# Performance work log

Measured on AMD Instinct MI355X. Metric: run time of the kernel, lower is better.

## Reference

```python
import jax, jax.numpy as jnp
import numpy as np

EPS = 1e-6
NEG = -1e9
RES_RATIO = 1.0  # res_ratio init arg
MAKE_SYM = True


def _ln(x, g, b):
    m = jnp.mean(x, axis=-1, keepdims=True)
    v = jnp.mean((x - m) ** 2, axis=-1, keepdims=True)
    return (x - m) * jax.lax.rsqrt(v + EPS) * g + b


def _sim(q, k, W1q, W1k, b1, W2, b2):
    # NN(concat([q,k])) with first dense split into query/key halves:
    # relu(q@W1q + k@W1k + b1) @ W2 + b2  -> avoids materializing the 2d concat.
    qa = q @ W1q  # [b,n,sq,h]
    kb = k @ W1k  # [b,n,sk,h]
    h1 = jax.nn.relu(qa[:, :, :, None, :] + kb[:, :, None, :, :] + b1)  # [b,n,sq,sk,h]
    s = jnp.einsum('bnqkh,h->bnqk', h1, W2[:, 0]) + b2[0]
    if MAKE_SYM:
        qb = q @ W1k
        ka = k @ W1q
        h2 = jax.nn.relu(ka[:, :, None, :, :] + qb[:, :, :, None, :] + b1)
        s = s + jnp.einsum('bnqkh,h->bnqk', h2, W2[:, 0]) + b2[0]
    return s


def _attention(v, k, q, mask, Ww, bw, Wd, bd, W1q, W1k, b1, W2, b2):
    q = q @ Ww + bw
    k = k @ Ww + bw
    v = v @ Ww + bw
    logits = _sim(q, k, W1q, W1k, b1, W2, b2)
    if mask is not None:
        logits = logits + mask * NEG
    attn = jax.nn.softmax(logits, axis=-1)
    out = jnp.einsum('bnqk,bnkd->bnqd', attn, v)
    return out @ Wd + bd, attn


def setup_inputs() -> dict:
    key = jax.random.key(0)
    B, N, S, D, DFF, H = 4, 1, 256, 128, 512, 128
    ks = jax.random.split(key, 16)
    s = 0.02
    inp = {
        'x': jax.random.normal(ks[0], (B, N, S, D), jnp.float32),
        'enc_output': jax.random.normal(ks[1], (B, N, S, D), jnp.float32),
        'com_mask': jnp.zeros((B, N, S, S), jnp.float32),
        'dec_mask': jnp.zeros((B, N, S, S), jnp.float32),
        # shared pairwise-score MLP NN: Dense(H, relu) -> Dense(1)
        'W1q': jax.random.normal(ks[2], (D, H), jnp.float32) * s,
        'W1k': jax.random.normal(ks[3], (D, H), jnp.float32) * s,
        'b1': jnp.zeros((H,), jnp.float32),
        'W2': jax.random.normal(ks[4], (H, 1), jnp.float32) * s,
        'b2': jnp.zeros((1,), jnp.float32),
        # mha1 projections
        'Ww1': jax.random.normal(ks[5], (D, D), jnp.float32) * s,
        'bw1': jnp.zeros((D,), jnp.float32),
        'Wd1': jax.random.normal(ks[6], (D, D), jnp.float32) * s,
        'bd1': jnp.zeros((D,), jnp.float32),
        # mha2 projections
        'Ww2': jax.random.normal(ks[7], (D, D), jnp.float32) * s,
        'bw2': jnp.zeros((D,), jnp.float32),
        'Wd2': jax.random.normal(ks[8], (D, D), jnp.float32) * s,
        'bd2': jnp.zeros((D,), jnp.float32),
        # ffn
        'Wf1': jax.random.normal(ks[9], (D, DFF), jnp.float32) * s,
        'bf1': jnp.zeros((DFF,), jnp.float32),
        'Wf2': jax.random.normal(ks[10], (DFF, D), jnp.float32) * s,
        'bf2': jnp.zeros((D,), jnp.float32),
        # layernorms
        'ln1_g': jnp.ones((D,), jnp.float32), 'ln1_b': jnp.zeros((D,), jnp.float32),
        'ln2_g': jnp.ones((D,), jnp.float32), 'ln2_b': jnp.zeros((D,), jnp.float32),
        'ln3_g': jnp.ones((D,), jnp.float32), 'ln3_b': jnp.zeros((D,), jnp.float32),
    }
    return inp


def reference(x, enc_output, com_mask, dec_mask,
              W1q, W1k, b1, W2, b2,
              Ww1, bw1, Wd1, bd1,
              Ww2, bw2, Wd2, bd2,
              Wf1, bf1, Wf2, bf2,
              ln1_g, ln1_b, ln2_g, ln2_b, ln3_g, ln3_b):
    r = RES_RATIO
    # self-attention block (dropout inactive, eval mode)
    attn1, aw1 = _attention(x, x, x, com_mask, Ww1, bw1, Wd1, bd1, W1q, W1k, b1, W2, b2)
    out1 = _ln((2 - r) * attn1 + r * x, ln1_g, ln1_b)
    # cross-attention block
    attn2, aw2 = _attention(enc_output, enc_output, out1, dec_mask, Ww2, bw2, Wd2, bd2, W1q, W1k, b1, W2, b2)
    out2 = _ln((2 - r) * attn2 + r * out1, ln2_g, ln2_b)
    # ffn
    ffn = jax.nn.relu(out2 @ Wf1 + bf1) @ Wf2 + bf2
    out3 = _ln((2 - r) * ffn + r * out2, ln3_g, ln3_b)
    return out3
```

## Files before the change

kernel.cpp:

```cpp
#include <hip/hip_runtime.h>
#include <math.h>


#define LN_EPS 1e-6f
#define NEGV  (-1e9f)

constexpr int B = 4, S = 256, D = 128, H = 128, DFF = 512;
constexpr int R = B * S;
constexpr int LDW = H + 4;

struct P {
    const float *x, *enc, *com_mask, *dec_mask;
    const float *W1q, *W1k, *b1, *W2;
    const float *Ww1, *bw1, *Wd1, *bd1;
    const float *Ww2, *bw2, *Wd2, *bd2;
    const float *Wf1, *bf1, *Wf2, *bf2;
    const float *ln1g, *ln1b, *ln2g, *ln2b, *ln3g, *ln3b;
    float *out;
    float *xw, *qa, *kb, *kv2w, *kb2, *ka2, *qa2, *qb2;
    float *sbuf, *sbuf2, *out1, *out2;
};

__device__ __forceinline__ float4 mm8(const float* AshS, const float* W,
                                      const float* bias, int lr, int c4)
{
    const float4* W4 = (const float4*)W;
    float4 acc = bias ? ((const float4*)bias)[c4] : make_float4(0.f, 0.f, 0.f, 0.f);
    #pragma unroll 8
    for (int k = 0; k < 128; ++k) {
        const float a = AshS[lr * 128 + k];
        const float4 w = W4[k * 32 + c4];
        acc.x = fmaf(a, w.x, acc.x); acc.y = fmaf(a, w.y, acc.y);
        acc.z = fmaf(a, w.z, acc.z); acc.w = fmaf(a, w.w, acc.w);
    }
    return acc;
}

__global__ __launch_bounds__(256) void proj3_kernel(P p)
{
    const int g = blockIdx.y, tid = threadIdx.x;
    const int r0 = blockIdx.x * 8;
    const int lr = tid >> 5, c4 = tid & 31;
    __shared__ float Ash[8 * 128];
    __shared__ float Pw[8 * 128];

    const float* A    = g ? p.enc  : p.x;
    const float* Wp   = g ? p.Ww2  : p.Ww1;
    const float* bp   = g ? p.bw2  : p.bw1;
    float*       o_w  = g ? p.kv2w : p.xw;
    const float* Wsec = g ? p.W1k  : p.W1q;
    const float* bsec = g ? nullptr: p.b1;
    float*       o_s  = g ? p.kb2  : p.qa;
    const float* Wthr = g ? p.W1q  : p.W1k;
    float*       o_t  = g ? p.ka2  : p.kb;

    ((float4*)Ash)[tid] = ((const float4*)(A + (size_t)r0 * 128))[tid];
    __syncthreads();
    {
        const float4 w = mm8(Ash, Wp, bp, lr, c4);
        ((float4*)(Pw + lr * 128))[c4] = w;
        ((float4*)o_w)[(size_t)(r0 + lr) * 32 + c4] = w;
    }
    __syncthreads();
    {
        const float4 q = mm8(Pw, Wsec, bsec, lr, c4);
        ((float4*)o_s)[(size_t)(r0 + lr) * 32 + c4] = q;
        const float4 k = mm8(Pw, Wthr, nullptr, lr, c4);
        ((float4*)o_t)[(size_t)(r0 + lr) * 32 + c4] = k;
    }
}

#define PW_STEP(AP0, AP1, BP0, BP1)                                            \
    {                                                                          \
        const float4 w  = *(const float4*)(W2s + h);                           \
        const float4 a0 = *(const float4*)((AP0) + h);                         \
        const float4 a1 = *(const float4*)((AP1) + h);                         \
        const float4 b0 = *(const float4*)((BP0) + h);                         \
        const float4 b1 = *(const float4*)((BP1) + h);                         \
        acc00 = fmaf(fmaxf(a0.x+b0.x,0.f),w.x,acc00); acc00 = fmaf(fmaxf(a0.y+b0.y,0.f),w.y,acc00); \
        acc00 = fmaf(fmaxf(a0.z+b0.z,0.f),w.z,acc00); acc00 = fmaf(fmaxf(a0.w+b0.w,0.f),w.w,acc00); \
        acc01 = fmaf(fmaxf(a0.x+b1.x,0.f),w.x,acc01); acc01 = fmaf(fmaxf(a0.y+b1.y,0.f),w.y,acc01); \
        acc01 = fmaf(fmaxf(a0.z+b1.z,0.f),w.z,acc01); acc01 = fmaf(fmaxf(a0.w+b1.w,0.f),w.w,acc01); \
        acc10 = fmaf(fmaxf(a1.x+b0.x,0.f),w.x,acc10); acc10 = fmaf(fmaxf(a1.y+b0.y,0.f),w.y,acc10); \
        acc10 = fmaf(fmaxf(a1.z+b0.z,0.f),w.z,acc10); acc10 = fmaf(fmaxf(a1.w+b0.w,0.f),w.w,acc10); \
        acc11 = fmaf(fmaxf(a1.x+b1.x,0.f),w.x,acc11); acc11 = fmaf(fmaxf(a1.y+b1.y,0.f),w.y,acc11); \
        acc11 = fmaf(fmaxf(a1.z+b1.z,0.f),w.z,acc11); acc11 = fmaf(fmaxf(a1.w+b1.w,0.f),w.w,acc11); \
    }

__global__ __launch_bounds__(256) void pairwise_self_kernel(P p)
{
    __shared__ __align__(16) float As[32 * LDW];
    __shared__ __align__(16) float Bs[32 * LDW];
    __shared__ __align__(16) float W2s[H];
    const int b = blockIdx.z, q0 = blockIdx.y * 32, k0 = blockIdx.x * 32;
    const int tid = threadIdx.x, bS = b * S;
    for (int i = tid; i < 32 * (H / 4); i += 256) {
        const int r = i >> 5, c4 = i & 31;
        ((float4*)(As + r * LDW))[c4] = ((const float4*)(p.qa + (size_t)(bS + q0 + r) * H))[c4];
        ((float4*)(Bs + r * LDW))[c4] = ((const float4*)(p.kb + (size_t)(bS + k0 + r) * H))[c4];
    }
    if (tid < H / 4) ((float4*)W2s)[tid] = ((const float4*)p.W2)[tid];
    __syncthreads();
    const int tx = tid & 15, ty = tid >> 4;
    const float* A0 = As + (2 * ty) * LDW; const float* A1 = A0 + LDW;
    const float* B0 = Bs + (2 * tx) * LDW; const float* B1 = B0 + LDW;
    float acc00 = 0.f, acc01 = 0.f, acc10 = 0.f, acc11 = 0.f;
    #pragma unroll 4
    for (int h = 0; h < H; h += 4) PW_STEP(A0, A1, B0, B1);
    const size_t base = (size_t)(bS + q0 + 2 * ty) * S + (k0 + 2 * tx);
    *(float2*)(p.sbuf + base)     = make_float2(acc00, acc01);
    *(float2*)(p.sbuf + base + S) = make_float2(acc10, acc11);
}

__global__ __launch_bounds__(256) void pairwise_cross2_kernel(P p)
{
    __shared__ __align__(16) float As[32 * LDW];
    __shared__ __align__(16) float Bs[32 * LDW];
    __shared__ __align__(16) float W2s[H];
    const int b = blockIdx.z, q0 = blockIdx.y * 32, k0 = blockIdx.x * 32;
    const int tid = threadIdx.x, bS = b * S;
    const int tx = tid & 15, ty = tid >> 4;
    const float* A0 = As + (2 * ty) * LDW; const float* A1 = A0 + LDW;
    const float* B0 = Bs + (2 * tx) * LDW; const float* B1 = B0 + LDW;
    float acc00 = 0.f, acc01 = 0.f, acc10 = 0.f, acc11 = 0.f;

    for (int i = tid; i < 32 * (H / 4); i += 256) {
        const int r = i >> 5, c4 = i & 31;
        ((float4*)(As + r * LDW))[c4] = ((const float4*)(p.qa2 + (size_t)(bS + q0 + r) * H))[c4];
        ((float4*)(Bs + r * LDW))[c4] = ((const float4*)(p.kb2 + (size_t)(bS + k0 + r) * H))[c4];
    }
    if (tid < H / 4) ((float4*)W2s)[tid] = ((const float4*)p.W2)[tid];
    __syncthreads();
    #pragma unroll 4
    for (int h = 0; h < H; h += 4) PW_STEP(A0, A1, B0, B1);
    __syncthreads();
    for (int i = tid; i < 32 * (H / 4); i += 256) {
        const int r = i >> 5, c4 = i & 31;
        ((float4*)(As + r * LDW))[c4] = ((const float4*)(p.qb2 + (size_t)(bS + q0 + r) * H))[c4];
        ((float4*)(Bs + r * LDW))[c4] = ((const float4*)(p.ka2 + (size_t)(bS + k0 + r) * H))[c4];
    }
    __syncthreads();
    #pragma unroll 4
    for (int h = 0; h < H; h += 4) PW_STEP(A0, A1, B0, B1);
    const size_t base = (size_t)(bS + q0 + 2 * ty) * S + (k0 + 2 * tx);
    *(float2*)(p.sbuf2 + base)     = make_float2(acc00, acc01);
    *(float2*)(p.sbuf2 + base + S) = make_float2(acc10, acc11);
}

template<bool SYM, bool QPROJ>
__global__ __launch_bounds__(256) void attn_tail_kernel(P p)
{
    __shared__ float s8[8 * 256];
    __shared__ float aoS[8 * 128];
    __shared__ float o1S[8 * 128];
    const float* Sin  = SYM ? p.sbuf : p.sbuf2;
    const float* mask = SYM ? p.com_mask : p.dec_mask;
    const float* V    = SYM ? p.xw : p.kv2w;
    const float* Wd   = SYM ? p.Wd1 : p.Wd2;
    const float* bd   = SYM ? p.bd1 : p.bd2;
    const float* res  = SYM ? p.x : p.out1;
    const float* lg   = SYM ? p.ln1g : p.ln2g;
    const float* lb   = SYM ? p.ln1b : p.ln2b;
    float* outp       = SYM ? p.out1 : p.out2;

    const int tid = threadIdx.x;
    const int r0 = blockIdx.x * 8, b = r0 >> 8, bS = b * S;

    for (int i = tid; i < 8 * 256; i += 256) {
        const int r = i >> 8, k = i & 255;
        const int row = r0 + r, q = row & 255;
        float l = Sin[(size_t)row * S + k];
        if (SYM) l += Sin[(size_t)(bS + k) * S + q];
        l += mask[(size_t)row * S + k] * NEGV;
        s8[i] = l;
    }
    __syncthreads();
    {
        const int g = tid >> 5, c = tid & 31;
        float* rowp = s8 + g * 256;
        float m = -INFINITY;
        for (int k = c; k < 256; k += 32) m = fmaxf(m, rowp[k]);
        for (int o = 16; o; o >>= 1) m = fmaxf(m, __shfl_xor(m, o, 32));
        float s = 0.f;
        for (int k = c; k < 256; k += 32) { const float e = __expf(rowp[k] - m); rowp[k] = e; s += e; }
        for (int o = 16; o; o >>= 1) s += __shfl_xor(s, o, 32);
        const float rinv = 1.f / s;
        for (int k = c; k < 256; k += 32) rowp[k] *= rinv;
    }
    __syncthreads();
    const int lr = tid >> 5, c4 = tid & 31;
    {
        const float4* V4 = (const float4*)(V + (size_t)bS * D);
        float4 acc = make_float4(0.f, 0.f, 0.f, 0.f);
        #pragma unroll 8
        for (int k = 0; k < 256; ++k) {
            const float a = s8[lr * 256 + k];
            const float4 v = V4[k * 32 + c4];
            acc.x = fmaf(a, v.x, acc.x); acc.y = fmaf(a, v.y, acc.y);
            acc.z = fmaf(a, v.z, acc.z); acc.w = fmaf(a, v.w, acc.w);
        }
        ((float4*)(aoS + lr * 128))[c4] = acc;
    }
    __syncthreads();
    {
        float4 o = mm8(aoS, Wd, bd, lr, c4);
        const float4 r4 = ((const float4*)(res + (size_t)(r0 + lr) * 128))[c4];
        const float x0 = o.x + r4.x, x1 = o.y + r4.y, x2 = o.z + r4.z, x3 = o.w + r4.w;
        float s  = x0 + x1 + x2 + x3;
        float s2 = x0 * x0 + x1 * x1 + x2 * x2 + x3 * x3;
        for (int of = 16; of; of >>= 1) { s += __shfl_xor(s, of, 32); s2 += __shfl_xor(s2, of, 32); }
        const float m = s * (1.f / 128), var = s2 * (1.f / 128) - m * m;
        const float rs = rsqrtf(var + LN_EPS);
        const float4 gv = ((const float4*)lg)[c4], bv = ((const float4*)lb)[c4];
        float4 o4;
        o4.x = (x0 - m) * rs * gv.x + bv.x; o4.y = (x1 - m) * rs * gv.y + bv.y;
        o4.z = (x2 - m) * rs * gv.z + bv.z; o4.w = (x3 - m) * rs * gv.w + bv.w;
        ((float4*)outp)[(size_t)(r0 + lr) * 32 + c4] = o4;
        if (QPROJ) { ((float4*)(o1S + lr * 128))[c4] = o4; }
    }
    if (QPROJ) {
        __syncthreads();
        const float4 w = mm8(o1S, p.Ww2, p.bw2, lr, c4);
        ((float4*)(aoS + lr * 128))[c4] = w;
        __syncthreads();
        const float4 q = mm8(aoS, p.W1q, p.b1, lr, c4);
        ((float4*)p.qa2)[(size_t)(r0 + lr) * 32 + c4] = q;
        const float4 k = mm8(aoS, p.W1k, p.b1, lr, c4);
        ((float4*)p.qb2)[(size_t)(r0 + lr) * 32 + c4] = k;
    }
}

__global__ __launch_bounds__(256) void ffn_kernel(P p)
{
    __shared__ float o2S[4 * 128];
    __shared__ float hidP[2 * 4 * 512];
    __shared__ float part[8 * 4 * 128];
    const int r0 = blockIdx.x * 4, tid = threadIdx.x;

    if (tid < 128) ((float4*)o2S)[tid] = ((const float4*)(p.out2 + (size_t)r0 * 128))[tid];
    __syncthreads();

    {
        const int c4 = tid & 127, kh = tid >> 7;
        const float4* Wf1_4 = (const float4*)p.Wf1;
        float4 a0 = make_float4(0.f,0.f,0.f,0.f), a1 = a0, a2 = a0, a3 = a0;
        const int kbase = kh * 64;
        #pragma unroll 8
        for (int k = 0; k < 64; ++k) {
            const int kk = kbase + k;
            const float4 w = Wf1_4[kk * 128 + c4];
            const float s0 = o2S[kk], s1 = o2S[128 + kk], s2 = o2S[256 + kk], s3 = o2S[384 + kk];
            a0.x = fmaf(s0, w.x, a0.x); a0.y = fmaf(s0, w.y, a0.y); a0.z = fmaf(s0, w.z, a0.z); a0.w = fmaf(s0, w.w, a0.w);
            a1.x = fmaf(s1, w.x, a1.x); a1.y = fmaf(s1, w.y, a1.y); a1.z = fmaf(s1, w.z, a1.z); a1.w = fmaf(s1, w.w, a1.w);
            a2.x = fmaf(s2, w.x, a2.x); a2.y = fmaf(s2, w.y, a2.y); a2.z = fmaf(s2, w.z, a2.z); a2.w = fmaf(s2, w.w, a2.w);
            a3.x = fmaf(s3, w.x, a3.x); a3.y = fmaf(s3, w.y, a3.y); a3.z = fmaf(s3, w.z, a3.z); a3.w = fmaf(s3, w.w, a3.w);
        }
        float4* h4 = (float4*)(hidP + kh * 2048);
        h4[0 * 128 + c4] = a0; h4[1 * 128 + c4] = a1;
        h4[2 * 128 + c4] = a2; h4[3 * 128 + c4] = a3;
    }
    __syncthreads();
    for (int i = tid; i < 2048; i += 256) {
        const int c = i & 511;
        hidP[i] = fmaxf(hidP[i] + hidP[2048 + i] + p.bf1[c], 0.f);
    }
    __syncthreads();

    {
        const int c4 = tid & 31, kg = tid >> 5;
        const float4* Wf2_4 = (const float4*)p.Wf2;
        float4 a0 = make_float4(0.f,0.f,0.f,0.f), a1 = a0, a2 = a0, a3 = a0;
        const int kbase = kg * 64;
        #pragma unroll 8
        for (int k = 0; k < 64; ++k) {
            const int kk = kbase + k;
            const float4 w = Wf2_4[kk * 32 + c4];
            const float s0 = hidP[kk], s1 = hidP[512 + kk], s2 = hidP[1024 + kk], s3 = hidP[1536 + kk];
            a0.x = fmaf(s0, w.x, a0.x); a0.y = fmaf(s0, w.y, a0.y); a0.z = fmaf(s0, w.z, a0.z); a0.w = fmaf(s0, w.w, a0.w);
            a1.x = fmaf(s1, w.x, a1.x); a1.y = fmaf(s1, w.y, a1.y); a1.z = fmaf(s1, w.z, a1.z); a1.w = fmaf(s1, w.w, a1.w);
            a2.x = fmaf(s2, w.x, a2.x); a2.y = fmaf(s2, w.y, a2.y); a2.z = fmaf(s2, w.z, a2.z); a2.w = fmaf(s2, w.w, a2.w);
            a3.x = fmaf(s3, w.x, a3.x); a3.y = fmaf(s3, w.y, a3.y); a3.z = fmaf(s3, w.z, a3.z); a3.w = fmaf(s3, w.w, a3.w);
        }
        float4* p4 = (float4*)part;
        p4[(kg * 4 + 0) * 32 + c4] = a0; p4[(kg * 4 + 1) * 32 + c4] = a1;
        p4[(kg * 4 + 2) * 32 + c4] = a2; p4[(kg * 4 + 3) * 32 + c4] = a3;
    }
    __syncthreads();

    if (tid < 128) {
        const int row = tid >> 5, c4 = tid & 31;
        const float4* p4 = (const float4*)part;
        float4 sum = ((const float4*)p.bf2)[c4];
        #pragma unroll
        for (int kg = 0; kg < 8; ++kg) {
            const float4 v = p4[(kg * 4 + row) * 32 + c4];
            sum.x += v.x; sum.y += v.y; sum.z += v.z; sum.w += v.w;
        }
        const float4 r4 = ((const float4*)o2S)[row * 32 + c4];
        const float x0 = sum.x + r4.x, x1 = sum.y + r4.y, x2 = sum.z + r4.z, x3 = sum.w + r4.w;
        float s  = x0 + x1 + x2 + x3;
        float s2 = x0 * x0 + x1 * x1 + x2 * x2 + x3 * x3;
        for (int of = 16; of; of >>= 1) { s += __shfl_xor(s, of, 32); s2 += __shfl_xor(s2, of, 32); }
        const float m = s * (1.f / 128), var = s2 * (1.f / 128) - m * m;
        const float rs = rsqrtf(var + LN_EPS);
        const float4 gv = ((const float4*)p.ln3g)[c4], bv = ((const float4*)p.ln3b)[c4];
        float4 o4;
        o4.x = (x0 - m) * rs * gv.x + bv.x; o4.y = (x1 - m) * rs * gv.y + bv.y;
        o4.z = (x2 - m) * rs * gv.z + bv.z; o4.w = (x3 - m) * rs * gv.w + bv.w;
        ((float4*)p.out)[(size_t)(r0 + row) * 32 + c4] = o4;
    }
}

extern "C" void kernel_launch(void* const* d_in, const int* in_sizes, int n_in,
                              void* d_out, int out_size, void* d_ws, size_t ws_size,
                              hipStream_t stream) {
    (void)in_sizes; (void)n_in; (void)out_size; (void)ws_size;
    P p;
    p.x        = (const float*)d_in[0];
    p.enc      = (const float*)d_in[1];
    p.com_mask = (const float*)d_in[2];
    p.dec_mask = (const float*)d_in[3];
    p.W1q = (const float*)d_in[4];
    p.W1k = (const float*)d_in[5];
    p.b1  = (const float*)d_in[6];
    p.W2  = (const float*)d_in[7];
    p.Ww1 = (const float*)d_in[9];
    p.bw1 = (const float*)d_in[10];
    p.Wd1 = (const float*)d_in[11];
    p.bd1 = (const float*)d_in[12];
    p.Ww2 = (const float*)d_in[13];
    p.bw2 = (const float*)d_in[14];
    p.Wd2 = (const float*)d_in[15];
    p.bd2 = (const float*)d_in[16];
    p.Wf1 = (const float*)d_in[17];
    p.bf1 = (const float*)d_in[18];
    p.Wf2 = (const float*)d_in[19];
    p.bf2 = (const float*)d_in[20];
    p.ln1g = (const float*)d_in[21];
    p.ln1b = (const float*)d_in[22];
    p.ln2g = (const float*)d_in[23];
    p.ln2b = (const float*)d_in[24];
    p.ln3g = (const float*)d_in[25];
    p.ln3b = (const float*)d_in[26];
    p.out  = (float*)d_out;

    float* ws = (float*)d_ws;
    const size_t RD  = (size_t)R * D;
    const size_t SSz = (size_t)B * S * S;
    p.xw    = ws;
    p.qa    = p.xw    + RD;
    p.kb    = p.qa    + RD;
    p.kv2w  = p.kb    + RD;
    p.kb2   = p.kv2w  + RD;
    p.ka2   = p.kb2   + RD;
    p.qa2   = p.ka2   + RD;
    p.qb2   = p.qa2   + RD;
    p.sbuf  = p.qb2   + RD;
    p.sbuf2 = p.sbuf  + SSz;
    p.out1  = p.sbuf2 + SSz;
    p.out2  = p.out1  + RD;

    proj3_kernel<<<dim3(R / 8, 2), 256, 0, stream>>>(p);
    pairwise_self_kernel<<<dim3(8, 8, 4), 256, 0, stream>>>(p);
    attn_tail_kernel<true, true><<<R / 8, 256, 0, stream>>>(p);
    pairwise_cross2_kernel<<<dim3(8, 8, 4), 256, 0, stream>>>(p);
    attn_tail_kernel<false, false><<<R / 8, 256, 0, stream>>>(p);
    ffn_kernel<<<R / 4, 256, 0, stream>>>(p);
}
```

Measured before the change: 199.0 us.

## Fuse pairwise scoring, softmax tail and FFN into per-row attention kernels

Merges the pairwise score kernels into the attention tail kernels, so each block of 8 query rows computes its logits against all 256 keys in shared memory. K tiles are register-prefetched one step ahead. The symmetric term is computed directly from the transposed projections rather than by reading the score transpose back from global memory, and the FFN plus its layernorm moves into the cross-attention kernel. This drops the score buffers and three launches. The catch is lower parallelism: 128 blocks, each recomputing against the full key set, with a small per-thread tile and no register blocking in the pairwise loop.

```diff
diff --git a/kernel.cpp b/kernel.cpp
--- a/kernel.cpp
+++ b/kernel.cpp
@@ -17,8 +17,7 @@
     const float *Wf1, *bf1, *Wf2, *bf2;
     const float *ln1g, *ln1b, *ln2g, *ln2b, *ln3g, *ln3b;
     float *out;
-    float *xw, *qa, *kb, *kv2w, *kb2, *ka2, *qa2, *qb2;
-    float *sbuf, *sbuf2, *out1, *out2;
+    float *xw, *qa, *kb, *kv2w, *kb2, *ka2, *qa2, *qb2, *out1;
 };
 
 __device__ __forceinline__ float4 mm8(const float* AshS, const float* W,
@@ -70,116 +69,106 @@
     }
 }
 
-#define PW_STEP(AP0, AP1, BP0, BP1)                                            \
-    {                                                                          \
-        const float4 w  = *(const float4*)(W2s + h);                           \
-        const float4 a0 = *(const float4*)((AP0) + h);                         \
-        const float4 a1 = *(const float4*)((AP1) + h);                         \
-        const float4 b0 = *(const float4*)((BP0) + h);                         \
-        const float4 b1 = *(const float4*)((BP1) + h);                         \
-        acc00 = fmaf(fmaxf(a0.x+b0.x,0.f),w.x,acc00); acc00 = fmaf(fmaxf(a0.y+b0.y,0.f),w.y,acc00); \
-        acc00 = fmaf(fmaxf(a0.z+b0.z,0.f),w.z,acc00); acc00 = fmaf(fmaxf(a0.w+b0.w,0.f),w.w,acc00); \
-        acc01 = fmaf(fmaxf(a0.x+b1.x,0.f),w.x,acc01); acc01 = fmaf(fmaxf(a0.y+b1.y,0.f),w.y,acc01); \
-        acc01 = fmaf(fmaxf(a0.z+b1.z,0.f),w.z,acc01); acc01 = fmaf(fmaxf(a0.w+b1.w,0.f),w.w,acc01); \
-        acc10 = fmaf(fmaxf(a1.x+b0.x,0.f),w.x,acc10); acc10 = fmaf(fmaxf(a1.y+b0.y,0.f),w.y,acc10); \
-        acc10 = fmaf(fmaxf(a1.z+b0.z,0.f),w.z,acc10); acc10 = fmaf(fmaxf(a1.w+b0.w,0.f),w.w,acc10); \
-        acc11 = fmaf(fmaxf(a1.x+b1.x,0.f),w.x,acc11); acc11 = fmaf(fmaxf(a1.y+b1.y,0.f),w.y,acc11); \
-        acc11 = fmaf(fmaxf(a1.z+b1.z,0.f),w.z,acc11); acc11 = fmaf(fmaxf(a1.w+b1.w,0.f),w.w,acc11); \
-    }
-
-__global__ __launch_bounds__(256) void pairwise_self_kernel(P p)
+template<bool CROSS>
+__global__ __launch_bounds__(256) void attn_fused(P p)
 {
-    __shared__ __align__(16) float As[32 * LDW];
-    __shared__ __align__(16) float Bs[32 * LDW];
-    __shared__ __align__(16) float W2s[H];
-    const int b = blockIdx.z, q0 = blockIdx.y * 32, k0 = blockIdx.x * 32;
-    const int tid = threadIdx.x, bS = b * S;
-    for (int i = tid; i < 32 * (H / 4); i += 256) {
-        const int r = i >> 5, c4 = i & 31;
-        ((float4*)(As + r * LDW))[c4] = ((const float4*)(p.qa + (size_t)(bS + q0 + r) * H))[c4];
-        ((float4*)(Bs + r * LDW))[c4] = ((const float4*)(p.kb + (size_t)(bS + k0 + r) * H))[c4];
-    }
-    if (tid < H / 4) ((float4*)W2s)[tid] = ((const float4*)p.W2)[tid];
-    __syncthreads();
-    const int tx = tid & 15, ty = tid >> 4;
-    const float* A0 = As + (2 * ty) * LDW; const float* A1 = A0 + LDW;
-    const float* B0 = Bs + (2 * tx) * LDW; const float* B1 = B0 + LDW;
-    float acc00 = 0.f, acc01 = 0.f, acc10 = 0.f, acc11 = 0.f;
-    #pragma unroll 4
-    for (int h = 0; h < H; h += 4) PW_STEP(A0, A1, B0, B1);
-    const size_t base = (size_t)(bS + q0 + 2 * ty) * S + (k0 + 2 * tx);
-    *(float2*)(p.sbuf + base)     = make_float2(acc00, acc01);
-    *(float2*)(p.sbuf + base + S) = make_float2(acc10, acc11);
-}
-
-__global__ __launch_bounds__(256) void pairwise_cross2_kernel(P p)
-{
-    __shared__ __align__(16) float As[32 * LDW];
-    __shared__ __align__(16) float Bs[32 * LDW];
-    __shared__ __align__(16) float W2s[H];
-    const int b = blockIdx.z, q0 = blockIdx.y * 32, k0 = blockIdx.x * 32;
-    const int tid = threadIdx.x, bS = b * S;
-    const int tx = tid & 15, ty = tid >> 4;
-    const float* A0 = As + (2 * ty) * LDW; const float* A1 = A0 + LDW;
-    const float* B0 = Bs + (2 * tx) * LDW; const float* B1 = B0 + LDW;
-    float acc00 = 0.f, acc01 = 0.f, acc10 = 0.f, acc11 = 0.f;
-
-    for (int i = tid; i < 32 * (H / 4); i += 256) {
-        const int r = i >> 5, c4 = i & 31;
-        ((float4*)(As + r * LDW))[c4] = ((const float4*)(p.qa2 + (size_t)(bS + q0 + r) * H))[c4];
-        ((float4*)(Bs + r * LDW))[c4] = ((const float4*)(p.kb2 + (size_t)(bS + k0 + r) * H))[c4];
-    }
-    if (tid < H / 4) ((float4*)W2s)[tid] = ((const float4*)p.W2)[tid];
-    __syncthreads();
-    #pragma unroll 4
-    for (int h = 0; h < H; h += 4) PW_STEP(A0, A1, B0, B1);
-    __syncthreads();
-    for (int i = tid; i < 32 * (H / 4); i += 256) {
-        const int r = i >> 5, c4 = i & 31;
-        ((float4*)(As + r * LDW))[c4] = ((const float4*)(p.qb2 + (size_t)(bS + q0 + r) * H))[c4];
-        ((float4*)(Bs + r * LDW))[c4] = ((const float4*)(p.ka2 + (size_t)(bS + k0 + r) * H))[c4];
-    }
-    __syncthreads();
-    #pragma unroll 4
-    for (int h = 0; h < H; h += 4) PW_STEP(A0, A1, B0, B1);
-    const size_t base = (size_t)(bS + q0 + 2 * ty) * S + (k0 + 2 * tx);
-    *(float2*)(p.sbuf2 + base)     = make_float2(acc00, acc01);
-    *(float2*)(p.sbuf2 + base + S) = make_float2(acc10, acc11);
-}
-
-template<bool SYM, bool QPROJ>
-__global__ __launch_bounds__(256) void attn_tail_kernel(P p)
-{
-    __shared__ float s8[8 * 256];
-    __shared__ float aoS[8 * 128];
-    __shared__ float o1S[8 * 128];
-    const float* Sin  = SYM ? p.sbuf : p.sbuf2;
-    const float* mask = SYM ? p.com_mask : p.dec_mask;
-    const float* V    = SYM ? p.xw : p.kv2w;
-    const float* Wd   = SYM ? p.Wd1 : p.Wd2;
-    const float* bd   = SYM ? p.bd1 : p.bd2;
-    const float* res  = SYM ? p.x : p.out1;
-    const float* lg   = SYM ? p.ln1g : p.ln2g;
-    const float* lb   = SYM ? p.ln1b : p.ln2b;
-    float* outp       = SYM ? p.out1 : p.out2;
+    __shared__ __align__(16) float smem[14784];
+    float* W2s  = smem;
+    float* Aq   = smem + 128;
+    float* Bq   = smem + 1184;
+    float* s8   = smem + 2240;
+    float* rowS = smem + 4288;
+    float* aoS  = smem + 5312;
+    float* Kt   = smem + 6336;
+    float* At   = smem + 10560;
 
     const int tid = threadIdx.x;
-    const int r0 = blockIdx.x * 8, b = r0 >> 8, bS = b * S;
-
-    for (int i = tid; i < 8 * 256; i += 256) {
-        const int r = i >> 8, k = i & 255;
-        const int row = r0 + r, q = row & 255;
-        float l = Sin[(size_t)row * S + k];
-        if (SYM) l += Sin[(size_t)(bS + k) * S + q];
-        l += mask[(size_t)row * S + k] * NEGV;
-        s8[i] = l;
-    }
-    __syncthreads();
+    const int r0 = blockIdx.x * 8, bS = r0 & ~(S - 1);
+
+    const float* Aq_src = CROSS ? p.qa2 : p.qa;
+    const float* Bq_src = CROSS ? p.qb2 : p.kb;
+    const float* Kt_src = CROSS ? p.kb2 : p.kb;
+    const float* At_src = CROSS ? p.ka2 : p.qa;
+    const float* mask   = CROSS ? p.dec_mask : p.com_mask;
+    const float* V      = CROSS ? p.kv2w : p.xw;
+    const float* Wd     = CROSS ? p.Wd2 : p.Wd1;
+    const float* bd     = CROSS ? p.bd2 : p.bd1;
+    const float* res    = CROSS ? p.out1 : p.x;
+    const float* lg     = CROSS ? p.ln2g : p.ln1g;
+    const float* lb     = CROSS ? p.ln2b : p.ln1b;
+
+    if (tid < 32) ((float4*)W2s)[tid] = ((const float4*)p.W2)[tid];
+    {
+        const int r = tid >> 5, c4 = tid & 31;
+        ((float4*)(Aq + r * LDW))[c4] = ((const float4*)(Aq_src + (size_t)(r0 + r) * H))[c4];
+        ((float4*)(Bq + r * LDW))[c4] = ((const float4*)(Bq_src + (size_t)(r0 + r) * H))[c4];
+    }
+
+    float4 pK[4], pA[4];
+    {
+        #pragma unroll
+        for (int j = 0; j < 4; ++j) {
+            const int i = tid + j * 256, r = i >> 5, c4 = i & 31;
+            pK[j] = ((const float4*)(Kt_src + (size_t)(bS + r) * H))[c4];
+            pA[j] = ((const float4*)(At_src + (size_t)(bS + r) * H))[c4];
+        }
+    }
+    const int q = tid >> 5, kk = tid & 31;
+    const float* aq = Aq + q * LDW;
+    const float* bq = Bq + q * LDW;
+    const float* kt = Kt + kk * LDW;
+    const float* at = At + kk * LDW;
+
+    for (int t = 0; t < 8; ++t) {
+        __syncthreads();
+        #pragma unroll
+        for (int j = 0; j < 4; ++j) {
+            const int i = tid + j * 256, r = i >> 5, c4 = i & 31;
+            ((float4*)(Kt + r * LDW))[c4] = pK[j];
+            ((float4*)(At + r * LDW))[c4] = pA[j];
+        }
+        __syncthreads();
+        if (t < 7) {
+            #pragma unroll
+            for (int j = 0; j < 4; ++j) {
+                const int i = tid + j * 256, r = i >> 5, c4 = i & 31;
+                pK[j] = ((const float4*)(Kt_src + (size_t)(bS + (t + 1) * 32 + r) * H))[c4];
+                pA[j] = ((const float4*)(At_src + (size_t)(bS + (t + 1) * 32 + r) * H))[c4];
+            }
+        }
+        float4 accA = make_float4(0.f, 0.f, 0.f, 0.f);
+        float4 accB = make_float4(0.f, 0.f, 0.f, 0.f);
+        #pragma unroll 8
+        for (int h = 0; h < H; h += 4) {
+            const float4 w  = *(const float4*)(W2s + h);
+            const float4 a  = *(const float4*)(aq + h);
+            const float4 k4 = *(const float4*)(kt + h);
+            const float4 b4 = *(const float4*)(bq + h);
+            const float4 a4 = *(const float4*)(at + h);
+            accA.x = fmaf(fmaxf(a.x + k4.x, 0.f), w.x, accA.x);
+            accA.y = fmaf(fmaxf(a.y + k4.y, 0.f), w.y, accA.y);
+            accA.z = fmaf(fmaxf(a.z + k4.z, 0.f), w.z, accA.z);
+            accA.w = fmaf(fmaxf(a.w + k4.w, 0.f), w.w, accA.w);
+            accB.x = fmaf(fmaxf(b4.x + a4.x, 0.f), w.x, accB.x);
+            accB.y = fmaf(fmaxf(b4.y + a4.y, 0.f), w.y, accB.y);
+            accB.z = fmaf(fmaxf(b4.z + a4.z, 0.f), w.z, accB.z);
+            accB.w = fmaf(fmaxf(b4.w + a4.w, 0.f), w.w, accB.w);
+        }
+        s8[q * 256 + t * 32 + kk] = (accA.x + accA.y + accA.z + accA.w)
+                                  + (accB.x + accB.y + accB.z + accB.w);
+    }
+    __syncthreads();
+
     {
         const int g = tid >> 5, c = tid & 31;
         float* rowp = s8 + g * 256;
+        const float* mrow = mask + (size_t)(r0 + g) * S;
         float m = -INFINITY;
-        for (int k = c; k < 256; k += 32) m = fmaxf(m, rowp[k]);
+        for (int k = c; k < 256; k += 32) {
+            const float v = rowp[k] + mrow[k] * NEGV;
+            rowp[k] = v;
+            m = fmaxf(m, v);
+        }
         for (int o = 16; o; o >>= 1) m = fmaxf(m, __shfl_xor(m, o, 32));
         float s = 0.f;
         for (int k = c; k < 256; k += 32) { const float e = __expf(rowp[k] - m); rowp[k] = e; s += e; }
@@ -188,6 +177,7 @@
         for (int k = c; k < 256; k += 32) rowp[k] *= rinv;
     }
     __syncthreads();
+
     const int lr = tid >> 5, c4 = tid & 31;
     {
         const float4* V4 = (const float4*)(V + (size_t)bS * D);
@@ -202,6 +192,7 @@
         ((float4*)(aoS + lr * 128))[c4] = acc;
     }
     __syncthreads();
+
     {
         float4 o = mm8(aoS, Wd, bd, lr, c4);
         const float4 r4 = ((const float4*)(res + (size_t)(r0 + lr) * 128))[c4];
@@ -215,99 +206,107 @@
         float4 o4;
         o4.x = (x0 - m) * rs * gv.x + bv.x; o4.y = (x1 - m) * rs * gv.y + bv.y;
         o4.z = (x2 - m) * rs * gv.z + bv.z; o4.w = (x3 - m) * rs * gv.w + bv.w;
-        ((float4*)outp)[(size_t)(r0 + lr) * 32 + c4] = o4;
-        if (QPROJ) { ((float4*)(o1S + lr * 128))[c4] = o4; }
-    }
-    if (QPROJ) {
-        __syncthreads();
-        const float4 w = mm8(o1S, p.Ww2, p.bw2, lr, c4);
+        ((float4*)(rowS + lr * 128))[c4] = o4;
+        if (!CROSS) ((float4*)p.out1)[(size_t)(r0 + lr) * 32 + c4] = o4;
+    }
+    __syncthreads();
+
+    if (!CROSS) {
+        const float4 w = mm8(rowS, p.Ww2, p.bw2, lr, c4);
+        __syncthreads();
         ((float4*)(aoS + lr * 128))[c4] = w;
         __syncthreads();
-        const float4 q = mm8(aoS, p.W1q, p.b1, lr, c4);
-        ((float4*)p.qa2)[(size_t)(r0 + lr) * 32 + c4] = q;
-        const float4 k = mm8(aoS, p.W1k, p.b1, lr, c4);
-        ((float4*)p.qb2)[(size_t)(r0 + lr) * 32 + c4] = k;
-    }
-}
-
-__global__ __launch_bounds__(256) void ffn_kernel(P p)
-{
-    __shared__ float o2S[4 * 128];
-    __shared__ float hidP[2 * 4 * 512];
-    __shared__ float part[8 * 4 * 128];
-    const int r0 = blockIdx.x * 4, tid = threadIdx.x;
-
-    if (tid < 128) ((float4*)o2S)[tid] = ((const float4*)(p.out2 + (size_t)r0 * 128))[tid];
-    __syncthreads();
-
-    {
-        const int c4 = tid & 127, kh = tid >> 7;
-        const float4* Wf1_4 = (const float4*)p.Wf1;
-        float4 a0 = make_float4(0.f,0.f,0.f,0.f), a1 = a0, a2 = a0, a3 = a0;
-        const int kbase = kh * 64;
-        #pragma unroll 8
-        for (int k = 0; k < 64; ++k) {
-            const int kk = kbase + k;
-            const float4 w = Wf1_4[kk * 128 + c4];
-            const float s0 = o2S[kk], s1 = o2S[128 + kk], s2 = o2S[256 + kk], s3 = o2S[384 + kk];
-            a0.x = fmaf(s0, w.x, a0.x); a0.y = fmaf(s0, w.y, a0.y); a0.z = fmaf(s0, w.z, a0.z); a0.w = fmaf(s0, w.w, a0.w);
-            a1.x = fmaf(s1, w.x, a1.x); a1.y = fmaf(s1, w.y, a1.y); a1.z = fmaf(s1, w.z, a1.z); a1.w = fmaf(s1, w.w, a1.w);
-            a2.x = fmaf(s2, w.x, a2.x); a2.y = fmaf(s2, w.y, a2.y); a2.z = fmaf(s2, w.z, a2.z); a2.w = fmaf(s2, w.w, a2.w);
-            a3.x = fmaf(s3, w.x, a3.x); a3.y = fmaf(s3, w.y, a3.y); a3.z = fmaf(s3, w.z, a3.z); a3.w = fmaf(s3, w.w, a3.w);
-        }
-        float4* h4 = (float4*)(hidP + kh * 2048);
-        h4[0 * 128 + c4] = a0; h4[1 * 128 + c4] = a1;
-        h4[2 * 128 + c4] = a2; h4[3 * 128 + c4] = a3;
-    }
-    __syncthreads();
-    for (int i = tid; i < 2048; i += 256) {
-        const int c = i & 511;
-        hidP[i] = fmaxf(hidP[i] + hidP[2048 + i] + p.bf1[c], 0.f);
-    }
-    __syncthreads();
-
-    {
-        const int c4 = tid & 31, kg = tid >> 5;
-        const float4* Wf2_4 = (const float4*)p.Wf2;
-        float4 a0 = make_float4(0.f,0.f,0.f,0.f), a1 = a0, a2 = a0, a3 = a0;
-        const int kbase = kg * 64;
-        #pragma unroll 8
-        for (int k = 0; k < 64; ++k) {
-            const int kk = kbase + k;
-            const float4 w = Wf2_4[kk * 32 + c4];
-            const float s0 = hidP[kk], s1 = hidP[512 + kk], s2 = hidP[1024 + kk], s3 = hidP[1536 + kk];
-            a0.x = fmaf(s0, w.x, a0.x); a0.y = fmaf(s0, w.y, a0.y); a0.z = fmaf(s0, w.z, a0.z); a0.w = fmaf(s0, w.w, a0.w);
-            a1.x = fmaf(s1, w.x, a1.x); a1.y = fmaf(s1, w.y, a1.y); a1.z = fmaf(s1, w.z, a1.z); a1.w = fmaf(s1, w.w, a1.w);
-            a2.x = fmaf(s2, w.x, a2.x); a2.y = fmaf(s2, w.y, a2.y); a2.z = fmaf(s2, w.z, a2.z); a2.w = fmaf(s2, w.w, a2.w);
-            a3.x = fmaf(s3, w.x, a3.x); a3.y = fmaf(s3, w.y, a3.y); a3.z = fmaf(s3, w.z, a3.z); a3.w = fmaf(s3, w.w, a3.w);
-        }
-        float4* p4 = (float4*)part;
-        p4[(kg * 4 + 0) * 32 + c4] = a0; p4[(kg * 4 + 1) * 32 + c4] = a1;
-        p4[(kg * 4 + 2) * 32 + c4] = a2; p4[(kg * 4 + 3) * 32 + c4] = a3;
-    }
-    __syncthreads();
-
-    if (tid < 128) {
-        const int row = tid >> 5, c4 = tid & 31;
-        const float4* p4 = (const float4*)part;
-        float4 sum = ((const float4*)p.bf2)[c4];
-        #pragma unroll
-        for (int kg = 0; kg < 8; ++kg) {
-            const float4 v = p4[(kg * 4 + row) * 32 + c4];
-            sum.x += v.x; sum.y += v.y; sum.z += v.z; sum.w += v.w;
-        }
-        const float4 r4 = ((const float4*)o2S)[row * 32 + c4];
-        const float x0 = sum.x + r4.x, x1 = sum.y + r4.y, x2 = sum.z + r4.z, x3 = sum.w + r4.w;
-        float s  = x0 + x1 + x2 + x3;
-        float s2 = x0 * x0 + x1 * x1 + x2 * x2 + x3 * x3;
-        for (int of = 16; of; of >>= 1) { s += __shfl_xor(s, of, 32); s2 += __shfl_xor(s2, of, 32); }
-        const float m = s * (1.f / 128), var = s2 * (1.f / 128) - m * m;
-        const float rs = rsqrtf(var + LN_EPS);
-        const float4 gv = ((const float4*)p.ln3g)[c4], bv = ((const float4*)p.ln3b)[c4];
-        float4 o4;
-        o4.x = (x0 - m) * rs * gv.x + bv.x; o4.y = (x1 - m) * rs * gv.y + bv.y;
-        o4.z = (x2 - m) * rs * gv.z + bv.z; o4.w = (x3 - m) * rs * gv.w + bv.w;
-        ((float4*)p.out)[(size_t)(r0 + row) * 32 + c4] = o4;
+        const float4 qv = mm8(aoS, p.W1q, p.b1, lr, c4);
+        ((float4*)p.qa2)[(size_t)(r0 + lr) * 32 + c4] = qv;
+        const float4 kv = mm8(aoS, p.W1k, p.b1, lr, c4);
+        ((float4*)p.qb2)[(size_t)(r0 + lr) * 32 + c4] = kv;
+    } else {
+        float* h1p = smem + 6336;
+        float* hid = smem + 6336;
+        float* p2  = smem + 10432;
+
+        {
+            const int c = tid & 127, kh = tid >> 7;
+            const float4* Wf1_4 = (const float4*)p.Wf1;
+            float4 a0 = make_float4(0.f,0.f,0.f,0.f), a1 = a0, a2 = a0, a3 = a0,
+                   a4 = a0, a5 = a0, a6 = a0, a7 = a0;
+            const int kbase = kh * 64;
+            #pragma unroll 8
+            for (int k = 0; k < 64; ++k) {
+                const int kkk = kbase + k;
+                const float4 w = Wf1_4[kkk * 128 + c];
+                const float s0 = rowS[kkk],       s1 = rowS[128 + kkk];
+                const float s2 = rowS[256 + kkk], s3 = rowS[384 + kkk];
+                const float s4 = rowS[512 + kkk], s5 = rowS[640 + kkk];
+                const float s6 = rowS[768 + kkk], s7 = rowS[896 + kkk];
+                a0.x=fmaf(s0,w.x,a0.x); a0.y=fmaf(s0,w.y,a0.y); a0.z=fmaf(s0,w.z,a0.z); a0.w=fmaf(s0,w.w,a0.w);
+                a1.x=fmaf(s1,w.x,a1.x); a1.y=fmaf(s1,w.y,a1.y); a1.z=fmaf(s1,w.z,a1.z); a1.w=fmaf(s1,w.w,a1.w);
+                a2.x=fmaf(s2,w.x,a2.x); a2.y=fmaf(s2,w.y,a2.y); a2.z=fmaf(s2,w.z,a2.z); a2.w=fmaf(s2,w.w,a2.w);
+                a3.x=fmaf(s3,w.x,a3.x); a3.y=fmaf(s3,w.y,a3.y); a3.z=fmaf(s3,w.z,a3.z); a3.w=fmaf(s3,w.w,a3.w);
+                a4.x=fmaf(s4,w.x,a4.x); a4.y=fmaf(s4,w.y,a4.y); a4.z=fmaf(s4,w.z,a4.z); a4.w=fmaf(s4,w.w,a4.w);
+                a5.x=fmaf(s5,w.x,a5.x); a5.y=fmaf(s5,w.y,a5.y); a5.z=fmaf(s5,w.z,a5.z); a5.w=fmaf(s5,w.w,a5.w);
+                a6.x=fmaf(s6,w.x,a6.x); a6.y=fmaf(s6,w.y,a6.y); a6.z=fmaf(s6,w.z,a6.z); a6.w=fmaf(s6,w.w,a6.w);
+                a7.x=fmaf(s7,w.x,a7.x); a7.y=fmaf(s7,w.y,a7.y); a7.z=fmaf(s7,w.z,a7.z); a7.w=fmaf(s7,w.w,a7.w);
+            }
+            float4* h4 = (float4*)h1p;
+            const int base = kh * 1024;
+            h4[base + 0*128 + c] = a0; h4[base + 1*128 + c] = a1;
+            h4[base + 2*128 + c] = a2; h4[base + 3*128 + c] = a3;
+            h4[base + 4*128 + c] = a4; h4[base + 5*128 + c] = a5;
+            h4[base + 6*128 + c] = a6; h4[base + 7*128 + c] = a7;
+        }
+        __syncthreads();
+        for (int i = tid; i < 4096; i += 256) {
+            hid[i] = fmaxf(h1p[i] + h1p[4096 + i] + p.bf1[i & 511], 0.f);
+        }
+        __syncthreads();
+        {
+            const int c4f = tid & 31, kg = (tid >> 5) & 3, rh = tid >> 7;
+            const float4* Wf2_4 = (const float4*)p.Wf2;
+            float4 a0 = make_float4(0.f,0.f,0.f,0.f), a1 = a0, a2 = a0, a3 = a0;
+            const int kbase = kg * 128;
+            const float* h0 = hid + (rh * 4 + 0) * 512 + kbase;
+            const float* h1 = hid + (rh * 4 + 1) * 512 + kbase;
+            const float* h2 = hid + (rh * 4 + 2) * 512 + kbase;
+            const float* h3 = hid + (rh * 4 + 3) * 512 + kbase;
+            #pragma unroll 8
+            for (int k = 0; k < 128; ++k) {
+                const float4 w = Wf2_4[(kbase + k) * 32 + c4f];
+                const float s0 = h0[k], s1 = h1[k], s2 = h2[k], s3 = h3[k];
+                a0.x=fmaf(s0,w.x,a0.x); a0.y=fmaf(s0,w.y,a0.y); a0.z=fmaf(s0,w.z,a0.z); a0.w=fmaf(s0,w.w,a0.w);
+                a1.x=fmaf(s1,w.x,a1.x); a1.y=fmaf(s1,w.y,a1.y); a1.z=fmaf(s1,w.z,a1.z); a1.w=fmaf(s1,w.w,a1.w);
+                a2.x=fmaf(s2,w.x,a2.x); a2.y=fmaf(s2,w.y,a2.y); a2.z=fmaf(s2,w.z,a2.z); a2.w=fmaf(s2,w.w,a2.w);
+                a3.x=fmaf(s3,w.x,a3.x); a3.y=fmaf(s3,w.y,a3.y); a3.z=fmaf(s3,w.z,a3.z); a3.w=fmaf(s3,w.w,a3.w);
+            }
+            float4* p4 = (float4*)p2;
+            p4[kg * 256 + (rh * 4 + 0) * 32 + c4f] = a0;
+            p4[kg * 256 + (rh * 4 + 1) * 32 + c4f] = a1;
+            p4[kg * 256 + (rh * 4 + 2) * 32 + c4f] = a2;
+            p4[kg * 256 + (rh * 4 + 3) * 32 + c4f] = a3;
+        }
+        __syncthreads();
+        {
+            const float4* p4 = (const float4*)p2;
+            float4 sum = ((const float4*)p.bf2)[c4];
+            #pragma unroll
+            for (int kg = 0; kg < 4; ++kg) {
+                const float4 v = p4[kg * 256 + lr * 32 + c4];
+                sum.x += v.x; sum.y += v.y; sum.z += v.z; sum.w += v.w;
+            }
+            const float4 r4 = ((const float4*)(rowS + lr * 128))[c4];
+            const float x0 = sum.x + r4.x, x1 = sum.y + r4.y;
+            const float x2 = sum.z + r4.z, x3 = sum.w + r4.w;
+            float s  = x0 + x1 + x2 + x3;
+            float s2 = x0 * x0 + x1 * x1 + x2 * x2 + x3 * x3;
+            for (int of = 16; of; of >>= 1) { s += __shfl_xor(s, of, 32); s2 += __shfl_xor(s2, of, 32); }
+            const float m = s * (1.f / 128), var = s2 * (1.f / 128) - m * m;
+            const float rs = rsqrtf(var + LN_EPS);
+            const float4 gv = ((const float4*)p.ln3g)[c4], bv = ((const float4*)p.ln3b)[c4];
+            float4 o4;
+            o4.x = (x0 - m) * rs * gv.x + bv.x; o4.y = (x1 - m) * rs * gv.y + bv.y;
+            o4.z = (x2 - m) * rs * gv.z + bv.z; o4.w = (x3 - m) * rs * gv.w + bv.w;
+            ((float4*)p.out)[(size_t)(r0 + lr) * 32 + c4] = o4;
+        }
     }
 }
 
@@ -345,25 +344,18 @@
     p.out  = (float*)d_out;
 
     float* ws = (float*)d_ws;
-    const size_t RD  = (size_t)R * D;
-    const size_t SSz = (size_t)B * S * S;
-    p.xw    = ws;
-    p.qa    = p.xw    + RD;
-    p.kb    = p.qa    + RD;
-    p.kv2w  = p.kb    + RD;
-    p.kb2   = p.kv2w  + RD;
-    p.ka2   = p.kb2   + RD;
-    p.qa2   = p.ka2   + RD;
-    p.qb2   = p.qa2   + RD;
-    p.sbuf  = p.qb2   + RD;
-    p.sbuf2 = p.sbuf  + SSz;
-    p.out1  = p.sbuf2 + SSz;
-    p.out2  = p.out1  + RD;
+    const size_t RD = (size_t)R * D;
+    p.xw   = ws;
+    p.qa   = p.xw   + RD;
+    p.kb   = p.qa   + RD;
+    p.kv2w = p.kb   + RD;
+    p.kb2  = p.kv2w + RD;
+    p.ka2  = p.kb2  + RD;
+    p.qa2  = p.ka2  + RD;
+    p.qb2  = p.qa2  + RD;
+    p.out1 = p.qb2  + RD;
 
     proj3_kernel<<<dim3(R / 8, 2), 256, 0, stream>>>(p);
-    pairwise_self_kernel<<<dim3(8, 8, 4), 256, 0, stream>>>(p);
-    attn_tail_kernel<true, true><<<R / 8, 256, 0, stream>>>(p);
-    pairwise_cross2_kernel<<<dim3(8, 8, 4), 256, 0, stream>>>(p);
-    attn_tail_kernel<false, false><<<R / 8, 256, 0, stream>>>(p);
-    ffn_kernel<<<R / 4, 256, 0, stream>>>(p);
+    attn_fused<false><<<R / 8, 256, 0, stream>>>(p);
+    attn_fused<true><<<R / 8, 256, 0, stream>>>(p);
 }
```

Measured after the change: 257.8 us. 1.3x slower.
